# Kernel tuning notes

Hardware: AMD Instinct MI355X
Metric: run time of the kernel (lower is better)

The kernel has to match this reference:

```python
import jax, jax.numpy as jnp
import numpy as np

ND, NT, B = 16384, 16384, 4096
FD, FT, C = 256, 256, 768


def _gat(x_src, x_dst, ei, Ws, Wd, a_s, a_d, b, num_dst, self_loops):
    """PyG GATConv, heads=1: per-edge attention softmax over incoming edges."""
    if self_loops:
        loops = jnp.arange(num_dst, dtype=ei.dtype)
        ei = jnp.concatenate([ei, jnp.stack([loops, loops])], axis=1)
    src, dst = ei[0], ei[1]
    hs = x_src @ Ws                                   # [Ns, C]
    hd = x_dst @ Wd                                   # [Ndst, C]
    e = jax.nn.leaky_relu((hs @ a_s)[src] + (hd @ a_d)[dst], 0.2)   # [E]
    m = jax.ops.segment_max(e, dst, num_segments=num_dst)
    p = jnp.exp(e - m[dst])
    s = jax.ops.segment_sum(p, dst, num_segments=num_dst)
    alpha = p / (s[dst] + 1e-16)
    out = jax.ops.segment_sum(hs[src] * alpha[:, None], dst, num_segments=num_dst)
    return out + b


def _l2norm(x):
    n = jnp.linalg.norm(x, axis=1, keepdims=True)
    return x / jnp.maximum(n, 1e-12)


def setup_inputs() -> dict:
    ks = iter(jax.random.split(jax.random.key(0), 64))
    def nrm(shape, fan_in=None):
        s = 1.0 if fan_in is None else (1.0 / fan_in) ** 0.5
        return jax.random.normal(next(ks), shape, jnp.float32) * s
    inp = {}
    inp["x_drug"] = nrm((ND, FD))
    inp["x_target"] = nrm((NT, FT))
    inp["cell_features"] = nrm((B, 890))
    for et, fs, fd in (("dd", FD, FD), ("dt", FD, FT), ("tt", FT, FT)):
        inp[f"W_src_{et}"] = nrm((fs, C), fs)
        inp[f"W_dst_{et}"] = nrm((fd, C), fd)
        inp[f"a_src_{et}"] = nrm((C,), C)
        inp[f"a_dst_{et}"] = nrm((C,), C)
        inp[f"b_{et}"] = jnp.zeros((C,), jnp.float32)
    for name, fi, fo in (("red1", 890, 2048), ("red2", 2048, 512), ("red3", 512, 2 * C),
                         ("r2a", 4 * C, 2048), ("r2b", 2048, 512), ("r2c", 512, C), ("cls", C, 2)):
        inp[f"{name}_w"] = nrm((fi, fo), fi)
        inp[f"{name}_b"] = jnp.zeros((fo,), jnp.float32)
    inp["drug1_id"] = jax.random.randint(next(ks), (B,), 0, ND)
    inp["drug2_id"] = jax.random.randint(next(ks), (B,), 0, ND)
    inp["ei_dd"] = jax.random.randint(next(ks), (2, 131072), 0, ND)
    inp["ei_dt"] = jnp.stack([jax.random.randint(next(ks), (262144,), 0, ND),
                              jax.random.randint(next(ks), (262144,), 0, NT)])
    inp["ei_tt"] = jax.random.randint(next(ks), (2, 262144), 0, NT)
    return inp


def reference(x_drug, x_target, cell_features,
              W_src_dd, W_dst_dd, a_src_dd, a_dst_dd, b_dd,
              W_src_dt, W_dst_dt, a_src_dt, a_dst_dt, b_dt,
              W_src_tt, W_dst_tt, a_src_tt, a_dst_tt, b_tt,
              red1_w, red1_b, red2_w, red2_b, red3_w, red3_b,
              r2a_w, r2a_b, r2b_w, r2b_b, r2c_w, r2c_b,
              cls_w, cls_b,
              drug1_id, drug2_id, ei_dd, ei_dt, ei_tt):
    # HeteroConv (aggr='sum') followed by per-type ReLU, num_layers=1
    drug = jax.nn.relu(_gat(x_drug, x_drug, ei_dd,
                            W_src_dd, W_dst_dd, a_src_dd, a_dst_dd, b_dd, ND, True))
    target = jax.nn.relu(
        _gat(x_drug, x_target, ei_dt, W_src_dt, W_dst_dt, a_src_dt, a_dst_dt, b_dt, NT, False)
        + _gat(x_target, x_target, ei_tt, W_src_tt, W_dst_tt, a_src_tt, a_dst_tt, b_tt, NT, True))
    del target  # with num_layers=1 the target embeddings never feed the output (faithful)
    d1 = drug[drug1_id]
    d2 = drug[drug2_id]
    cell = _l2norm(cell_features)
    cell = jax.nn.relu(cell @ red1_w + red1_b)
    cell = jax.nn.relu(cell @ red2_w + red2_b)
    cell = jax.nn.relu(cell @ red3_w + red3_b)          # [B, 2*C]
    hidden = _l2norm(jnp.concatenate([d1, d2, cell], axis=1))  # [B, 4*C]
    hidden = jax.nn.relu(hidden @ r2a_w + r2a_b)
    hidden = jax.nn.relu(hidden @ r2b_w + r2b_b)
    hidden = jax.nn.relu(hidden @ r2c_w + r2c_b)
    return hidden @ cls_w + cls_b                       # [B, 2]
```

## Files before the change

kernel.cpp:

```cpp
#include <hip/hip_runtime.h>
#include <cstdint>

#define ND 16384
#define BATCH 4096
#define CDIM 768
#define E_DD 131072
#define FD 256

typedef unsigned short u16;
typedef u16 u16x4 __attribute__((ext_vector_type(4)));
typedef u16 u16x8 __attribute__((ext_vector_type(8)));
typedef short s16x8 __attribute__((ext_vector_type(8)));
typedef float f32x4 __attribute__((ext_vector_type(4)));

__device__ __forceinline__ u16 f2bf(float x) {
  union { float f; uint32_t u; } v; v.f = x;
  uint32_t r = v.u + 0x7fffu + ((v.u >> 16) & 1u);
  return (u16)(r >> 16);
}
__device__ __forceinline__ float bf2f(u16 h) {
  union { float f; uint32_t u; } v; v.u = ((uint32_t)h) << 16;
  return v.f;
}
__device__ __forceinline__ uint32_t split2p(float x) {
  u16 h = f2bf(x);
  u16 l = f2bf(x - bf2f(h));
  return ((uint32_t)h << 16) | l;
}

#define GLOAD_LDS16(gp, lp)                                                   \
  __builtin_amdgcn_global_load_lds(                                           \
      (__attribute__((address_space(1))) void*)(gp),                          \
      (__attribute__((address_space(3))) void*)(lp), 16, 0, 0)

#define KP 40

template <int KS, int OUT_BF16, int RELU, int BIAS, int ASPLIT, int ALO, int BLO,
          int BKD>
__device__ __forceinline__ void gemm_core(
    int bx, int by, int bz,
    const float* __restrict__ Af,
    const u16* __restrict__ Ahi, const u16* __restrict__ Alo,
    const u16* __restrict__ Bhi, const u16* __restrict__ Blo,
    const float* __restrict__ bias,
    float* __restrict__ Cf, u16* __restrict__ Chi,
    int M, int N, int K, u16* AsB, u16* BsB) {
  constexpr int MT = 4, NT = 4;
  constexpr int BM = 128, BN = 128;
  constexpr int ASEG = BM / 64;
  constexpr int BSEG = BN / 64;
  constexpr bool DIRECT = (ASPLIT == 0 && ALO == 0 && BLO == 0);

  const int t = threadIdx.x;
  const int bm0 = bx * BM, bn0 = by * BN;
  const int wid = t >> 6, lane = t & 63;
  const int quad = lane >> 4, l16 = lane & 15;
  const int wm0 = (wid >> 1) * (MT * 16);
  const int wn0 = (wid & 1) * (NT * 16);

  const int chunk = K / KS;
  const int kbeg = (KS > 1) ? bz * chunk : 0;
  const int kend = kbeg + chunk;

  f32x4 acc[MT][NT];
#pragma unroll
  for (int i = 0; i < MT; ++i)
#pragma unroll
    for (int j = 0; j < NT; ++j) acc[i][j] = (f32x4){0.f, 0.f, 0.f, 0.f};

  if constexpr (DIRECT) {
    constexpr int SLOTS = BKD / 8;
    constexpr int SM = SLOTS - 1;
    constexpr int NLD = (BM * BKD) / (256 * 8);
    auto stageA = [&](int buf, int kk) {
#pragma unroll
      for (int c = 0; c < NLD; ++c) {
        int s = t + 256 * c;
        int r = s / SLOTS, j = s % SLOTS;
        int jj = j ^ (r & SM);
        size_t goff = (size_t)(bm0 + r) * K + kk + jj * 8;
        int lofs = __builtin_amdgcn_readfirstlane((wid * 64 + 256 * c) * 8);
        GLOAD_LDS16(Ahi + goff, AsB + buf * (BM * BKD) + lofs);
      }
    };
    auto stageB = [&](int buf, int kk) {
#pragma unroll
      for (int c = 0; c < NLD; ++c) {
        int s = t + 256 * c;
        int r = s / SLOTS, j = s % SLOTS;
        int jj = j ^ (r & SM);
        size_t goff = (size_t)(bn0 + r) * K + kk + jj * 8;
        int lofs = __builtin_amdgcn_readfirstlane((wid * 64 + 256 * c) * 8);
        GLOAD_LDS16(Bhi + goff, BsB + buf * (BN * BKD) + lofs);
      }
    };
    stageA(0, kbeg);
    stageB(0, kbeg);
    const int rsw = l16 & SM;
    int cur = 0;
    for (int k0 = kbeg;;) {
      __syncthreads();
      int kn = k0 + BKD;
      if (kn < kend) {
        stageA(cur ^ 1, kn);
        stageB(cur ^ 1, kn);
      }
      const u16* Ab = AsB + cur * (BM * BKD);
      const u16* Bb = BsB + cur * (BN * BKD);
#pragma unroll
      for (int h = 0; h < BKD / 32; ++h) {
        s16x8 ah[MT], bh[NT];
#pragma unroll
        for (int mi = 0; mi < MT; ++mi)
          ah[mi] = *(const s16x8*)(Ab + (wm0 + mi * 16 + l16) * BKD +
                                   (((h * 4 + quad) ^ rsw) * 8));
#pragma unroll
        for (int ni = 0; ni < NT; ++ni)
          bh[ni] = *(const s16x8*)(Bb + (wn0 + ni * 16 + l16) * BKD +
                                   (((h * 4 + quad) ^ rsw) * 8));
#pragma unroll
        for (int mi = 0; mi < MT; ++mi)
#pragma unroll
          for (int ni = 0; ni < NT; ++ni)
            acc[mi][ni] = __builtin_amdgcn_mfma_f32_16x16x32_bf16(
                ah[mi], bh[ni], acc[mi][ni], 0, 0, 0);
      }
      k0 = kn;
      cur ^= 1;
      if (k0 >= kend) break;
    }
  } else {
    auto As = [&](int a, int r, int k) -> u16& { return AsB[(a * BM + r) * KP + k]; };
    auto Bs = [&](int a, int r, int k) -> u16& { return BsB[(a * BN + r) * KP + k]; };

    u16x8 pAh[ASEG], pAl[ASEG], pBh[BSEG], pBl[BSEG];

    auto loadA = [&](int c, int kk) {
      int s = t + 256 * c, row = s >> 2, kq = (s & 3) * 8;
      size_t off = (size_t)(bm0 + row) * K + kk + kq;
      if (ASPLIT) {
        f32x4 v0 = *(const f32x4*)(Af + off);
        f32x4 v1 = *(const f32x4*)(Af + off + 4);
        u16x8 h, l;
#pragma unroll
        for (int e = 0; e < 4; ++e) {
          uint32_t p = split2p(v0[e]);
          h[e] = (u16)(p >> 16); l[e] = (u16)(p & 0xffffu);
          uint32_t q = split2p(v1[e]);
          h[e + 4] = (u16)(q >> 16); l[e + 4] = (u16)(q & 0xffffu);
        }
        pAh[c] = h; pAl[c] = l;
      } else {
        pAh[c] = *(const u16x8*)(Ahi + off);
        if (ALO) pAl[c] = *(const u16x8*)(Alo + off);
      }
    };
    auto loadB = [&](int c, int kk) {
      int s = t + 256 * c, row = s >> 2, kq = (s & 3) * 8;
      size_t off = (size_t)(bn0 + row) * K + kk + kq;
      pBh[c] = *(const u16x8*)(Bhi + off);
      if (BLO) pBl[c] = *(const u16x8*)(Blo + off);
    };

#pragma unroll
    for (int c = 0; c < ASEG; ++c) loadA(c, kbeg);
#pragma unroll
    for (int c = 0; c < BSEG; ++c) loadB(c, kbeg);

    for (int k0 = kbeg;;) {
      __syncthreads();
#pragma unroll
      for (int c = 0; c < ASEG; ++c) {
        int s = t + 256 * c, row = s >> 2, kq = (s & 3) * 8;
        *(u16x8*)&As(0, row, kq) = pAh[c];
        if (ALO) *(u16x8*)&As(1, row, kq) = pAl[c];
      }
#pragma unroll
      for (int c = 0; c < BSEG; ++c) {
        int s = t + 256 * c, row = s >> 2, kq = (s & 3) * 8;
        *(u16x8*)&Bs(0, row, kq) = pBh[c];
        if (BLO) *(u16x8*)&Bs(1, row, kq) = pBl[c];
      }
      __syncthreads();

      int kn = k0 + 32;
      if (kn < kend) {
#pragma unroll
        for (int c = 0; c < ASEG; ++c) loadA(c, kn);
#pragma unroll
        for (int c = 0; c < BSEG; ++c) loadB(c, kn);
      }

      s16x8 ah[MT], al[MT], bh[NT], bl[NT];
#pragma unroll
      for (int mi = 0; mi < MT; ++mi) {
        ah[mi] = *(const s16x8*)&As(0, wm0 + mi * 16 + l16, quad * 8);
        if (ALO) al[mi] = *(const s16x8*)&As(1, wm0 + mi * 16 + l16, quad * 8);
      }
#pragma unroll
      for (int ni = 0; ni < NT; ++ni) {
        bh[ni] = *(const s16x8*)&Bs(0, wn0 + ni * 16 + l16, quad * 8);
        if (BLO) bl[ni] = *(const s16x8*)&Bs(1, wn0 + ni * 16 + l16, quad * 8);
      }
#pragma unroll
      for (int mi = 0; mi < MT; ++mi)
#pragma unroll
        for (int ni = 0; ni < NT; ++ni) {
          acc[mi][ni] = __builtin_amdgcn_mfma_f32_16x16x32_bf16(
              ah[mi], bh[ni], acc[mi][ni], 0, 0, 0);
          if (BLO)
            acc[mi][ni] = __builtin_amdgcn_mfma_f32_16x16x32_bf16(
                ah[mi], bl[ni], acc[mi][ni], 0, 0, 0);
          if (ALO)
            acc[mi][ni] = __builtin_amdgcn_mfma_f32_16x16x32_bf16(
                al[mi], bh[ni], acc[mi][ni], 0, 0, 0);
        }
      k0 = kn;
      if (k0 >= kend) break;
    }
  }

  float* Cp = (KS > 1) ? Cf + (size_t)bz * M * N : Cf;
#pragma unroll
  for (int mi = 0; mi < MT; ++mi) {
#pragma unroll
    for (int ni = 0; ni < NT; ++ni) {
      int row = bm0 + wm0 + mi * 16 + quad * 4;
      int col = bn0 + wn0 + ni * 16 + l16;
      float bv = BIAS ? bias[col] : 0.f;
#pragma unroll
      for (int r = 0; r < 4; ++r) {
        float v = acc[mi][ni][r] + bv;
        if (RELU) v = fmaxf(v, 0.f);
        size_t o = (size_t)(row + r) * N + col;
        if (OUT_BF16) Chi[o] = f2bf(v);
        else Cp[o] = v;
      }
    }
  }
}

template <int KS, int OUT_BF16, int RELU, int BIAS, int ASPLIT, int ALO, int BLO,
          int BKD>
__global__ __launch_bounds__(256) void mfma_gemm(
    const float* __restrict__ Af,
    const u16* __restrict__ Ahi, const u16* __restrict__ Alo,
    const u16* __restrict__ Bhi, const u16* __restrict__ Blo,
    const float* __restrict__ bias,
    float* __restrict__ Cf, u16* __restrict__ Chi,
    int M, int N, int K) {
  constexpr bool DIRECT = (ASPLIT == 0 && ALO == 0 && BLO == 0);
  __shared__ __align__(16) u16 AsB[DIRECT ? 2 * 128 * BKD : (ALO ? 2 : 1) * 128 * KP];
  __shared__ __align__(16) u16 BsB[DIRECT ? 2 * 128 * BKD : (BLO ? 2 : 1) * 128 * KP];
  gemm_core<KS, OUT_BF16, RELU, BIAS, ASPLIT, ALO, BLO, BKD>(
      blockIdx.x, blockIdx.y, (KS > 1) ? (int)blockIdx.z : 0,
      Af, Ahi, Alo, Bhi, Blo, bias, Cf, Chi, M, N, K, AsB, BsB);
}

__global__ __launch_bounds__(256) void dual_gemm_red1_hs(
    const u16* __restrict__ cn, const u16* __restrict__ r1T,
    const float* __restrict__ red1_b, u16* __restrict__ c1,
    const float* __restrict__ xd, const u16* __restrict__ wsrcT,
    u16* __restrict__ hs) {
  __shared__ __align__(16) u16 SMEM[16384];
  int b = blockIdx.x;
  if (b < 512) {
    gemm_core<1, 1, 1, 1, 0, 0, 0, 32>(b & 31, b >> 5, 0, nullptr, cn, nullptr,
                                       r1T, nullptr, red1_b, nullptr, c1,
                                       BATCH, 2048, 896, SMEM, SMEM + 2 * 128 * 32);
  } else {
    int b2 = b - 512;
    gemm_core<1, 1, 0, 0, 1, 1, 0, 32>(b2 & 127, b2 >> 7, 0, xd, nullptr, nullptr,
                                       wsrcT, nullptr, nullptr, nullptr, hs,
                                       ND, CDIM, FD, SMEM, SMEM + 2 * 128 * KP);
  }
}

template <int KS>
__global__ void reduce_split_ks(const float* __restrict__ P,
                                const float* __restrict__ bias,
                                u16* __restrict__ Chi, int M, int N) {
  int i = blockIdx.x * 256 + threadIdx.x;
  int total = (M * N) >> 2;
  if (i >= total) return;
  f32x4 s = ((const f32x4*)P)[i];
#pragma unroll
  for (int z = 1; z < KS; ++z) s += ((const f32x4*)P)[(size_t)z * total + i];
  int col = (i * 4) % N;
  f32x4 bv = *(const f32x4*)(bias + col);
  u16x4 h;
#pragma unroll
  for (int e = 0; e < 4; ++e) h[e] = f2bf(fmaxf(s[e] + bv[e], 0.f));
  *(u16x4*)&Chi[i * 4] = h;
}

__global__ void reduce_cls(const float* __restrict__ P,
                           const float* __restrict__ bias,
                           const float* __restrict__ clsw,
                           const float* __restrict__ clsb,
                           float* __restrict__ out) {
  int row = blockIdx.x * 4 + (threadIdx.x >> 6);
  int lane = threadIdx.x & 63;
  const f32x4* p0 = (const f32x4*)(P + (size_t)row * CDIM);
  const f32x4* p1 = (const f32x4*)(P + (size_t)BATCH * CDIM + (size_t)row * CDIM);
  float s0 = 0.f, s1 = 0.f;
#pragma unroll
  for (int i = 0; i < 3; ++i) {
    int c4 = lane + 64 * i;
    f32x4 a = p0[c4] + p1[c4];
    f32x4 bv = *(const f32x4*)(bias + c4 * 4);
#pragma unroll
    for (int e = 0; e < 4; ++e) {
      float h = fmaxf(a[e] + bv[e], 0.f);
      int c = c4 * 4 + e;
      s0 = fmaf(h, clsw[c * 2 + 0], s0);
      s1 = fmaf(h, clsw[c * 2 + 1], s1);
    }
  }
#pragma unroll
  for (int m = 32; m; m >>= 1) {
    s0 += __shfl_xor(s0, m);
    s1 += __shfl_xor(s1, m);
  }
  if (lane == 0) {
    out[row * 2 + 0] = s0 + clsb[0];
    out[row * 2 + 1] = s1 + clsb[1];
  }
}

struct TDesc {
  const float* W;
  u16* Th;
  int K, N, Kpad, start;
};
struct TPack { TDesc d[7]; };

__global__ void multi_transpose(TPack p) {
  __shared__ float tile[32][33];
  int b = blockIdx.x;
  int mi = 0;
#pragma unroll
  for (int i = 1; i < 7; ++i)
    if (b >= p.d[i].start) mi = i;
  TDesc dd = p.d[mi];
  int rel = b - dd.start;
  int tilesX = dd.Kpad / 32;
  int k0 = (rel % tilesX) * 32, n0 = (rel / tilesX) * 32;
  int tx = threadIdx.x, ty = threadIdx.y;
#pragma unroll
  for (int i = 0; i < 4; ++i) {
    int k = k0 + ty + 8 * i, n = n0 + tx;
    tile[ty + 8 * i][tx] = (k < dd.K && n < dd.N) ? dd.W[(size_t)k * dd.N + n] : 0.f;
  }
  __syncthreads();
#pragma unroll
  for (int i = 0; i < 4; ++i) {
    int n = n0 + ty + 8 * i, k = k0 + tx;
    if (n < dd.N) dd.Th[(size_t)n * dd.Kpad + k] = f2bf(tile[tx][ty + 8 * i]);
  }
}

__global__ void wvec_kernel(const float* __restrict__ Wsrc,
                            const float* __restrict__ Wdst,
                            const float* __restrict__ a_s,
                            const float* __restrict__ a_d,
                            float* __restrict__ wsv, float* __restrict__ wdv) {
  int k = blockIdx.x;
  int t = threadIdx.x;
  __shared__ float rs[256], rd[256];
  float s = 0.f, d = 0.f;
  for (int c = t; c < CDIM; c += 256) {
    s += Wsrc[(size_t)k * CDIM + c] * a_s[c];
    d += Wdst[(size_t)k * CDIM + c] * a_d[c];
  }
  rs[t] = s; rd[t] = d;
  __syncthreads();
  for (int st = 128; st; st >>= 1) {
    if (t < st) { rs[t] += rs[t + st]; rd[t] += rd[t + st]; }
    __syncthreads();
  }
  if (t == 0) { wsv[k] = rs[0]; wdv[k] = rd[0]; }
}

__global__ void esed_kernel(const float* __restrict__ x,
                            const float* __restrict__ wsv,
                            const float* __restrict__ wdv,
                            float* __restrict__ es, float* __restrict__ ed) {
  int i = blockIdx.x * 256 + threadIdx.x;
  int lane = threadIdx.x & 63;
  int row = i >> 6;
  int c4 = lane * 4;
  f32x4 v = ((const f32x4*)x)[i];
  f32x4 ws = *(const f32x4*)(wsv + c4);
  f32x4 wd = *(const f32x4*)(wdv + c4);
  float a = v[0] * ws[0] + v[1] * ws[1] + v[2] * ws[2] + v[3] * ws[3];
  float b = v[0] * wd[0] + v[1] * wd[1] + v[2] * wd[2] + v[3] * wd[3];
#pragma unroll
  for (int m = 32; m; m >>= 1) {
    a += __shfl_xor(a, m);
    b += __shfl_xor(b, m);
  }
  if (lane == 0) { es[row] = a; ed[row] = b; }
}

__global__ void init_csr(int* counts, int* mask, int* cnt) {
  int i = blockIdx.x * 256 + threadIdx.x;
  if (i < ND) { counts[i] = 1; mask[i] = 0; }
  if (i == 0) *cnt = 0;
}
__global__ void mark_kernel(const int* __restrict__ d1, const int* __restrict__ d2,
                            int* mask) {
  int i = blockIdx.x * 256 + threadIdx.x;
  if (i < BATCH) {
    mask[d1[i]] = 1;
    mask[d2[i]] = 1;
  }
}
__global__ void compact_kernel(const int* __restrict__ mask, int* cnt, int* list) {
  int i = blockIdx.x * 256 + threadIdx.x;
  if (i < ND && mask[i]) {
    int pos = atomicAdd(cnt, 1);
    list[pos] = i;
  }
}

__global__ void count_edges(const int* __restrict__ dst, int* counts) {
  int e = blockIdx.x * 256 + threadIdx.x;
  if (e < E_DD) atomicAdd(&counts[dst[e]], 1);
}
__global__ void scan_kernel(const int* __restrict__ counts, int* __restrict__ offsets,
                            int* __restrict__ cursor, int* __restrict__ slots) {
  __shared__ int part[512];
  int t = threadIdx.x;
  int base = t * 32;
  int s = 0;
  for (int i = 0; i < 32; ++i) s += counts[base + i];
  part[t] = s;
  __syncthreads();
  if (t == 0) {
    int run = 0;
    for (int i = 0; i < 512; ++i) { int tmp = part[i]; part[i] = run; run += tmp; }
    offsets[ND] = run;
  }
  __syncthreads();
  int run = part[t];
  for (int i = 0; i < 32; ++i) {
    int d = base + i;
    offsets[d] = run;
    slots[run] = d;
    cursor[d] = run + 1;
    run += counts[d];
  }
}
__global__ void scatter_edges(const int* __restrict__ src, const int* __restrict__ dst,
                              int* cursor, int* slots) {
  int e = blockIdx.x * 256 + threadIdx.x;
  if (e < E_DD) {
    int pos = atomicAdd(&cursor[dst[e]], 1);
    slots[pos] = src[e];
  }
}

__global__ __launch_bounds__(256) void gat_aggregate(
    const u16* __restrict__ hs, const float* __restrict__ es,
    const float* __restrict__ ed, const int* __restrict__ offsets,
    const int* __restrict__ slots, const float* __restrict__ bias,
    const int* __restrict__ list, const int* __restrict__ cnt,
    u16* __restrict__ out) {
  int idx = blockIdx.x * 4 + (threadIdx.x >> 6);
  if (idx >= *cnt) return;
  int d = list[idx];
  int lane = threadIdx.x & 63;
  int beg = offsets[d], end = offsets[d + 1];
  float edv = ed[d];
  float mx = -1e30f;
  for (int j = beg + lane; j < end; j += 64) {
    float e = es[slots[j]] + edv;
    e = e >= 0.f ? e : 0.2f * e;
    mx = fmaxf(mx, e);
  }
#pragma unroll
  for (int m = 32; m; m >>= 1) mx = fmaxf(mx, __shfl_xor(mx, m));
  float sm = 0.f;
  for (int j = beg + lane; j < end; j += 64) {
    float e = es[slots[j]] + edv;
    e = e >= 0.f ? e : 0.2f * e;
    sm += expf(e - mx);
  }
#pragma unroll
  for (int m = 32; m; m >>= 1) sm += __shfl_xor(sm, m);
  float inv = 1.f / (sm + 1e-16f);
  int c8 = lane * 8;
  int c4 = 512 + lane * 4;
  float a8[8] = {};
  float a4[4] = {};
  for (int j = beg; j < end; ++j) {
    int srcn = slots[j];
    float e = es[srcn] + edv;
    e = e >= 0.f ? e : 0.2f * e;
    float alpha = expf(e - mx) * inv;
    const u16* hrow = hs + (size_t)srcn * CDIM;
    u16x8 r8 = *(const u16x8*)(hrow + c8);
    u16x4 r4 = *(const u16x4*)(hrow + c4);
#pragma unroll
    for (int e2 = 0; e2 < 8; ++e2) a8[e2] = fmaf(alpha, bf2f(r8[e2]), a8[e2]);
#pragma unroll
    for (int e2 = 0; e2 < 4; ++e2) a4[e2] = fmaf(alpha, bf2f(r4[e2]), a4[e2]);
  }
  u16* orow = out + (size_t)d * CDIM;
  u16x8 o8;
  u16x4 o4;
#pragma unroll
  for (int e2 = 0; e2 < 8; ++e2) o8[e2] = f2bf(fmaxf(a8[e2] + bias[c8 + e2], 0.f));
#pragma unroll
  for (int e2 = 0; e2 < 4; ++e2) o4[e2] = f2bf(fmaxf(a4[e2] + bias[c4 + e2], 0.f));
  *(u16x8*)(orow + c8) = o8;
  *(u16x4*)(orow + c4) = o4;
}

__global__ void l2norm_bf16(const float* __restrict__ in, u16* __restrict__ hi,
                            int L, int Lp) {
  int row = blockIdx.x;
  int t = threadIdx.x;
  __shared__ float red[256];
  const float* irow = in + (size_t)row * L;
  float s = 0.f;
  for (int c = t; c < L; c += 256) { float v = irow[c]; s += v * v; }
  red[t] = s;
  __syncthreads();
  for (int st = 128; st; st >>= 1) {
    if (t < st) red[t] += red[t + st];
    __syncthreads();
  }
  float inv = 1.f / fmaxf(sqrtf(red[0]), 1e-12f);
  for (int c = t; c < Lp; c += 256) {
    float v = (c < L) ? irow[c] * inv : 0.f;
    hi[(size_t)row * Lp + c] = f2bf(v);
  }
}

__global__ __launch_bounds__(256) void hidden_build_bf16(
    const u16* __restrict__ drug, const u16* __restrict__ c3,
    const int* __restrict__ d1, const int* __restrict__ d2,
    u16* __restrict__ hhi) {
  int row = blockIdx.x;
  int t = threadIdx.x;
  const u16* s1 = drug + (size_t)d1[row] * CDIM;
  const u16* s2 = drug + (size_t)d2[row] * CDIM;
  const u16* s3 = c3 + (size_t)row * (2 * CDIM);
  float vals[12];
  float ss = 0.f;
#pragma unroll
  for (int i = 0; i < 12; ++i) {
    int c = t + 256 * i;
    float v;
    if (i < 3)      v = bf2f(s1[c]);
    else if (i < 6) v = bf2f(s2[c - CDIM]);
    else            v = bf2f(s3[c - 2 * CDIM]);
    vals[i] = v;
    ss += v * v;
  }
  __shared__ float red[256];
  red[t] = ss;
  __syncthreads();
  for (int st = 128; st; st >>= 1) {
    if (t < st) red[t] += red[t + st];
    __syncthreads();
  }
  float inv = 1.f / fmaxf(sqrtf(red[0]), 1e-12f);
  u16* hrow_h = hhi + (size_t)row * (4 * CDIM);
#pragma unroll
  for (int i = 0; i < 12; ++i) hrow_h[t + 256 * i] = f2bf(vals[i] * inv);
}

extern "C" void kernel_launch(void* const* d_in, const int* in_sizes, int n_in,
                              void* d_out, int out_size, void* d_ws, size_t ws_size,
                              hipStream_t stream) {
  const float* x_drug   = (const float*)d_in[0];
  const float* cellf    = (const float*)d_in[2];
  const float* W_src_dd = (const float*)d_in[3];
  const float* W_dst_dd = (const float*)d_in[4];
  const float* a_src_dd = (const float*)d_in[5];
  const float* a_dst_dd = (const float*)d_in[6];
  const float* b_dd     = (const float*)d_in[7];
  const float* red1_w = (const float*)d_in[18];
  const float* red1_b = (const float*)d_in[19];
  const float* red2_w = (const float*)d_in[20];
  const float* red2_b = (const float*)d_in[21];
  const float* red3_w = (const float*)d_in[22];
  const float* red3_b = (const float*)d_in[23];
  const float* r2a_w  = (const float*)d_in[24];
  const float* r2a_b  = (const float*)d_in[25];
  const float* r2b_w  = (const float*)d_in[26];
  const float* r2b_b  = (const float*)d_in[27];
  const float* r2c_w  = (const float*)d_in[28];
  const float* r2c_b  = (const float*)d_in[29];
  const float* cls_w  = (const float*)d_in[30];
  const float* cls_b  = (const float*)d_in[31];
  const int* drug1_id = (const int*)d_in[32];
  const int* drug2_id = (const int*)d_in[33];
  const int* ei_dd    = (const int*)d_in[34];
  float* out = (float*)d_out;

  const int* dd_src = ei_dd;
  const int* dd_dst = ei_dd + E_DD;

  char* w = (char*)d_ws;
  size_t off = 0;
  auto alloc = [&](size_t bytes) -> char* {
    char* p = w + off;
    off = (off + bytes + 255) & ~(size_t)255;
    return p;
  };
  u16* hs   = (u16*)alloc((size_t)ND * CDIM * 2);
  u16* drug = (u16*)alloc((size_t)ND * CDIM * 2);
  u16* c3   = (u16*)alloc((size_t)BATCH * 2 * CDIM * 2);
  float* P  = (float*)alloc((size_t)4 * BATCH * 512 * 4);
  u16* hid_hi = hs;
  u16* cn_hi = (u16*)alloc((size_t)BATCH * 896 * 2);
  u16* c1_hi = (u16*)alloc((size_t)BATCH * 2048 * 2);
  u16* c2_hi = (u16*)alloc((size_t)BATCH * 512 * 2);
  u16* wsrcT_hi = (u16*)alloc((size_t)CDIM * FD * 2);
  u16* r1T_hi = (u16*)alloc((size_t)2048 * 896 * 2);
  u16* r2T_hi = (u16*)alloc((size_t)512 * 2048 * 2);
  u16* r3T_hi = (u16*)alloc((size_t)1536 * 512 * 2);
  u16* raT_hi = (u16*)alloc((size_t)2048 * 3072 * 2);
  u16* rbT_hi = (u16*)alloc((size_t)512 * 2048 * 2);
  u16* rcT_hi = (u16*)alloc((size_t)768 * 512 * 2);
  float* es  = (float*)alloc((size_t)ND * 4);
  float* ed  = (float*)alloc((size_t)ND * 4);
  float* wsv = (float*)alloc(FD * 4);
  float* wdv = (float*)alloc(FD * 4);
  int* counts  = (int*)alloc((size_t)ND * 4);
  int* offsets = (int*)alloc((size_t)(ND + 1) * 4);
  int* cursor  = (int*)alloc((size_t)ND * 4);
  int* slots   = (int*)alloc((size_t)(E_DD + ND) * 4);
  int* mask    = (int*)alloc((size_t)ND * 4);
  int* list    = (int*)alloc((size_t)ND * 4);
  int* cnt     = (int*)alloc(256);
  (void)ws_size; (void)n_in; (void)in_sizes; (void)out_size;

  TPack tp;
  tp.d[0] = {W_src_dd, wsrcT_hi, 256, 768, 256, 0};
  tp.d[1] = {red1_w, r1T_hi, 890, 2048, 896, 192};
  tp.d[2] = {red2_w, r2T_hi, 2048, 512, 2048, 1984};
  tp.d[3] = {red3_w, r3T_hi, 512, 1536, 512, 3008};
  tp.d[4] = {r2a_w, raT_hi, 3072, 2048, 3072, 3776};
  tp.d[5] = {r2b_w, rbT_hi, 2048, 512, 2048, 9920};
  tp.d[6] = {r2c_w, rcT_hi, 512, 768, 512, 10944};
  multi_transpose<<<11328, dim3(32, 8), 0, stream>>>(tp);

  wvec_kernel<<<FD, 256, 0, stream>>>(W_src_dd, W_dst_dd, a_src_dd, a_dst_dd, wsv, wdv);
  esed_kernel<<<ND * FD / 1024, 256, 0, stream>>>(x_drug, wsv, wdv, es, ed);
  init_csr<<<ND / 256, 256, 0, stream>>>(counts, mask, cnt);
  mark_kernel<<<BATCH / 256, 256, 0, stream>>>(drug1_id, drug2_id, mask);
  compact_kernel<<<ND / 256, 256, 0, stream>>>(mask, cnt, list);
  l2norm_bf16<<<BATCH, 256, 0, stream>>>(cellf, cn_hi, 890, 896);

  dual_gemm_red1_hs<<<1280, 256, 0, stream>>>(cn_hi, r1T_hi, red1_b, c1_hi,
                                              x_drug, wsrcT_hi, hs);

  mfma_gemm<4, 0, 0, 0, 0, 0, 0, 64><<<dim3(BATCH / 128, 512 / 128, 4), 256, 0, stream>>>(
      nullptr, c1_hi, nullptr, r2T_hi, nullptr, nullptr, P, nullptr, BATCH, 512, 2048);
  reduce_split_ks<4><<<BATCH * 512 / 1024, 256, 0, stream>>>(P, red2_b, c2_hi, BATCH, 512);
  mfma_gemm<1, 1, 1, 1, 0, 0, 0, 64><<<dim3(BATCH / 128, 1536 / 128), 256, 0, stream>>>(
      nullptr, c2_hi, nullptr, r3T_hi, nullptr, red3_b, nullptr, c3, BATCH, 1536, 512);

  count_edges<<<E_DD / 256, 256, 0, stream>>>(dd_dst, counts);
  scan_kernel<<<1, 512, 0, stream>>>(counts, offsets, cursor, slots);
  scatter_edges<<<E_DD / 256, 256, 0, stream>>>(dd_src, dd_dst, cursor, slots);
  gat_aggregate<<<ND / 4, 256, 0, stream>>>(hs, es, ed, offsets, slots, b_dd, list, cnt, drug);

  hidden_build_bf16<<<BATCH, 256, 0, stream>>>(drug, c3, drug1_id, drug2_id, hid_hi);

  mfma_gemm<1, 1, 1, 1, 0, 0, 0, 64><<<dim3(BATCH / 128, 2048 / 128), 256, 0, stream>>>(
      nullptr, hid_hi, nullptr, raT_hi, nullptr, r2a_b, nullptr, c1_hi, BATCH, 2048, 3072);
  mfma_gemm<4, 0, 0, 0, 0, 0, 0, 64><<<dim3(BATCH / 128, 512 / 128, 4), 256, 0, stream>>>(
      nullptr, c1_hi, nullptr, rbT_hi, nullptr, nullptr, P, nullptr, BATCH, 512, 2048);
  reduce_split_ks<4><<<BATCH * 512 / 1024, 256, 0, stream>>>(P, r2b_b, c2_hi, BATCH, 512);
  mfma_gemm<2, 0, 0, 0, 0, 0, 0, 64><<<dim3(BATCH / 128, CDIM / 128, 2), 256, 0, stream>>>(
      nullptr, c2_hi, nullptr, rcT_hi, nullptr, nullptr, P, nullptr, BATCH, CDIM, 512);
  reduce_cls<<<BATCH / 4, 256, 0, stream>>>(P, r2c_b, cls_w, cls_b, out);
}
```

Before: 461.3 us.

## Add 4-stage counted-vmcnt LDS pipeline for direct bf16 GEMMs

Adds a 4-buffer, BK=32 pipeline path to the direct-load MFMA GEMM. It issues three stages ahead and waits with explicit s_waitcnt vmcnt counts instead of a full __syncthreads drain, so global-to-LDS loads overlap compute more deeply. All standalone dense GEMM launches switch from 2x64 to 4x32 buffering, keeping LDS size the same. Bias loads are also hoisted before the main loop. The hand-counted vmcnt depends on the exact number of loads each stage issues, which makes it fragile, and the smaller K step means more barriers per tile.

```diff
diff --git a/kernel.cpp b/kernel.cpp
--- a/kernel.cpp
+++ b/kernel.cpp
@@ -36,7 +36,7 @@
 #define KP 40
 
 template <int KS, int OUT_BF16, int RELU, int BIAS, int ASPLIT, int ALO, int BLO,
-          int BKD>
+          int BKD, int NBUF>
 __device__ __forceinline__ void gemm_core(
     int bx, int by, int bz,
     const float* __restrict__ Af,
@@ -62,6 +62,11 @@
   const int kbeg = (KS > 1) ? bz * chunk : 0;
   const int kend = kbeg + chunk;
 
+  float bvv[NT];
+#pragma unroll
+  for (int ni = 0; ni < NT; ++ni)
+    bvv[ni] = BIAS ? bias[bn0 + wn0 + ni * 16 + l16] : 0.f;
+
   f32x4 acc[MT][NT];
 #pragma unroll
   for (int i = 0; i < MT; ++i)
@@ -94,30 +99,71 @@
         GLOAD_LDS16(Bhi + goff, BsB + buf * (BN * BKD) + lofs);
       }
     };
-    stageA(0, kbeg);
-    stageB(0, kbeg);
     const int rsw = l16 & SM;
-    int cur = 0;
-    for (int k0 = kbeg;;) {
-      __syncthreads();
-      int kn = k0 + BKD;
-      if (kn < kend) {
-        stageA(cur ^ 1, kn);
-        stageB(cur ^ 1, kn);
-      }
-      const u16* Ab = AsB + cur * (BM * BKD);
-      const u16* Bb = BsB + cur * (BN * BKD);
-#pragma unroll
-      for (int h = 0; h < BKD / 32; ++h) {
+
+    if constexpr (NBUF == 2) {
+      stageA(0, kbeg);
+      stageB(0, kbeg);
+      int cur = 0;
+      for (int k0 = kbeg;;) {
+        __syncthreads();
+        int kn = k0 + BKD;
+        if (kn < kend) {
+          stageA(cur ^ 1, kn);
+          stageB(cur ^ 1, kn);
+        }
+        const u16* Ab = AsB + cur * (BM * BKD);
+        const u16* Bb = BsB + cur * (BN * BKD);
+#pragma unroll
+        for (int h = 0; h < BKD / 32; ++h) {
+          s16x8 ah[MT], bh[NT];
+#pragma unroll
+          for (int mi = 0; mi < MT; ++mi)
+            ah[mi] = *(const s16x8*)(Ab + (wm0 + mi * 16 + l16) * BKD +
+                                     (((h * 4 + quad) ^ rsw) * 8));
+#pragma unroll
+          for (int ni = 0; ni < NT; ++ni)
+            bh[ni] = *(const s16x8*)(Bb + (wn0 + ni * 16 + l16) * BKD +
+                                     (((h * 4 + quad) ^ rsw) * 8));
+#pragma unroll
+          for (int mi = 0; mi < MT; ++mi)
+#pragma unroll
+            for (int ni = 0; ni < NT; ++ni)
+              acc[mi][ni] = __builtin_amdgcn_mfma_f32_16x16x32_bf16(
+                  ah[mi], bh[ni], acc[mi][ni], 0, 0, 0);
+        }
+        k0 = kn;
+        cur ^= 1;
+        if (k0 >= kend) break;
+      }
+    } else {
+      static_assert(NBUF == 4 && BKD == 32, "counted path assumes 4x32");
+      const int nt = (kend - kbeg) / BKD;
+      stageA(0, kbeg);            stageB(0, kbeg);
+      stageA(1, kbeg + BKD);      stageB(1, kbeg + BKD);
+      stageA(2, kbeg + 2 * BKD);  stageB(2, kbeg + 2 * BKD);
+      for (int i = 0; i < nt; ++i) {
+        if (i <= nt - 3)      asm volatile("s_waitcnt vmcnt(8)" ::: "memory");
+        else if (i == nt - 2) asm volatile("s_waitcnt vmcnt(4)" ::: "memory");
+        else                  asm volatile("s_waitcnt vmcnt(0)" ::: "memory");
+        __builtin_amdgcn_s_barrier();
+        __builtin_amdgcn_sched_barrier(0);
+        if (i + 3 < nt) {
+          int b = (i + 3) & 3, kk = kbeg + (i + 3) * BKD;
+          stageA(b, kk);
+          stageB(b, kk);
+        }
+        const u16* Ab = AsB + (i & 3) * (BM * BKD);
+        const u16* Bb = BsB + (i & 3) * (BM * BKD);
         s16x8 ah[MT], bh[NT];
 #pragma unroll
         for (int mi = 0; mi < MT; ++mi)
           ah[mi] = *(const s16x8*)(Ab + (wm0 + mi * 16 + l16) * BKD +
-                                   (((h * 4 + quad) ^ rsw) * 8));
+                                   ((quad ^ rsw) * 8));
 #pragma unroll
         for (int ni = 0; ni < NT; ++ni)
           bh[ni] = *(const s16x8*)(Bb + (wn0 + ni * 16 + l16) * BKD +
-                                   (((h * 4 + quad) ^ rsw) * 8));
+                                   ((quad ^ rsw) * 8));
 #pragma unroll
         for (int mi = 0; mi < MT; ++mi)
 #pragma unroll
@@ -125,9 +171,6 @@
             acc[mi][ni] = __builtin_amdgcn_mfma_f32_16x16x32_bf16(
                 ah[mi], bh[ni], acc[mi][ni], 0, 0, 0);
       }
-      k0 = kn;
-      cur ^= 1;
-      if (k0 >= kend) break;
     }
   } else {
     auto As = [&](int a, int r, int k) -> u16& { return AsB[(a * BM + r) * KP + k]; };
@@ -227,10 +270,9 @@
     for (int ni = 0; ni < NT; ++ni) {
       int row = bm0 + wm0 + mi * 16 + quad * 4;
       int col = bn0 + wn0 + ni * 16 + l16;
-      float bv = BIAS ? bias[col] : 0.f;
 #pragma unroll
       for (int r = 0; r < 4; ++r) {
-        float v = acc[mi][ni][r] + bv;
+        float v = acc[mi][ni][r] + bvv[ni];
         if (RELU) v = fmaxf(v, 0.f);
         size_t o = (size_t)(row + r) * N + col;
         if (OUT_BF16) Chi[o] = f2bf(v);
@@ -241,7 +283,7 @@
 }
 
 template <int KS, int OUT_BF16, int RELU, int BIAS, int ASPLIT, int ALO, int BLO,
-          int BKD>
+          int BKD, int NBUF>
 __global__ __launch_bounds__(256) void mfma_gemm(
     const float* __restrict__ Af,
     const u16* __restrict__ Ahi, const u16* __restrict__ Alo,
@@ -250,9 +292,9 @@
     float* __restrict__ Cf, u16* __restrict__ Chi,
     int M, int N, int K) {
   constexpr bool DIRECT = (ASPLIT == 0 && ALO == 0 && BLO == 0);
-  __shared__ __align__(16) u16 AsB[DIRECT ? 2 * 128 * BKD : (ALO ? 2 : 1) * 128 * KP];
-  __shared__ __align__(16) u16 BsB[DIRECT ? 2 * 128 * BKD : (BLO ? 2 : 1) * 128 * KP];
-  gemm_core<KS, OUT_BF16, RELU, BIAS, ASPLIT, ALO, BLO, BKD>(
+  __shared__ __align__(16) u16 AsB[DIRECT ? NBUF * 128 * BKD : (ALO ? 2 : 1) * 128 * KP];
+  __shared__ __align__(16) u16 BsB[DIRECT ? NBUF * 128 * BKD : (BLO ? 2 : 1) * 128 * KP];
+  gemm_core<KS, OUT_BF16, RELU, BIAS, ASPLIT, ALO, BLO, BKD, NBUF>(
       blockIdx.x, blockIdx.y, (KS > 1) ? (int)blockIdx.z : 0,
       Af, Ahi, Alo, Bhi, Blo, bias, Cf, Chi, M, N, K, AsB, BsB);
 }
@@ -265,14 +307,14 @@
   __shared__ __align__(16) u16 SMEM[16384];
   int b = blockIdx.x;
   if (b < 512) {
-    gemm_core<1, 1, 1, 1, 0, 0, 0, 32>(b & 31, b >> 5, 0, nullptr, cn, nullptr,
-                                       r1T, nullptr, red1_b, nullptr, c1,
-                                       BATCH, 2048, 896, SMEM, SMEM + 2 * 128 * 32);
+    gemm_core<1, 1, 1, 1, 0, 0, 0, 32, 2>(b & 31, b >> 5, 0, nullptr, cn, nullptr,
+                                          r1T, nullptr, red1_b, nullptr, c1,
+                                          BATCH, 2048, 896, SMEM, SMEM + 2 * 128 * 32);
   } else {
     int b2 = b - 512;
-    gemm_core<1, 1, 0, 0, 1, 1, 0, 32>(b2 & 127, b2 >> 7, 0, xd, nullptr, nullptr,
-                                       wsrcT, nullptr, nullptr, nullptr, hs,
-                                       ND, CDIM, FD, SMEM, SMEM + 2 * 128 * KP);
+    gemm_core<1, 1, 0, 0, 1, 1, 0, 32, 2>(b2 & 127, b2 >> 7, 0, xd, nullptr, nullptr,
+                                          wsrcT, nullptr, nullptr, nullptr, hs,
+                                          ND, CDIM, FD, SMEM, SMEM + 2 * 128 * KP);
   }
 }
 
@@ -660,10 +702,10 @@
   dual_gemm_red1_hs<<<1280, 256, 0, stream>>>(cn_hi, r1T_hi, red1_b, c1_hi,
                                               x_drug, wsrcT_hi, hs);
 
-  mfma_gemm<4, 0, 0, 0, 0, 0, 0, 64><<<dim3(BATCH / 128, 512 / 128, 4), 256, 0, stream>>>(
+  mfma_gemm<4, 0, 0, 0, 0, 0, 0, 32, 4><<<dim3(BATCH / 128, 512 / 128, 4), 256, 0, stream>>>(
       nullptr, c1_hi, nullptr, r2T_hi, nullptr, nullptr, P, nullptr, BATCH, 512, 2048);
   reduce_split_ks<4><<<BATCH * 512 / 1024, 256, 0, stream>>>(P, red2_b, c2_hi, BATCH, 512);
-  mfma_gemm<1, 1, 1, 1, 0, 0, 0, 64><<<dim3(BATCH / 128, 1536 / 128), 256, 0, stream>>>(
+  mfma_gemm<1, 1, 1, 1, 0, 0, 0, 32, 4><<<dim3(BATCH / 128, 1536 / 128), 256, 0, stream>>>(
       nullptr, c2_hi, nullptr, r3T_hi, nullptr, red3_b, nullptr, c3, BATCH, 1536, 512);
 
   count_edges<<<E_DD / 256, 256, 0, stream>>>(dd_dst, counts);
@@ -673,12 +715,12 @@
 
   hidden_build_bf16<<<BATCH, 256, 0, stream>>>(drug, c3, drug1_id, drug2_id, hid_hi);
 
-  mfma_gemm<1, 1, 1, 1, 0, 0, 0, 64><<<dim3(BATCH / 128, 2048 / 128), 256, 0, stream>>>(
+  mfma_gemm<1, 1, 1, 1, 0, 0, 0, 32, 4><<<dim3(BATCH / 128, 2048 / 128), 256, 0, stream>>>(
       nullptr, hid_hi, nullptr, raT_hi, nullptr, r2a_b, nullptr, c1_hi, BATCH, 2048, 3072);
-  mfma_gemm<4, 0, 0, 0, 0, 0, 0, 64><<<dim3(BATCH / 128, 512 / 128, 4), 256, 0, stream>>>(
+  mfma_gemm<4, 0, 0, 0, 0, 0, 0, 32, 4><<<dim3(BATCH / 128, 512 / 128, 4), 256, 0, stream>>>(
       nullptr, c1_hi, nullptr, rbT_hi, nullptr, nullptr, P, nullptr, BATCH, 512, 2048);
   reduce_split_ks<4><<<BATCH * 512 / 1024, 256, 0, stream>>>(P, r2b_b, c2_hi, BATCH, 512);
-  mfma_gemm<2, 0, 0, 0, 0, 0, 0, 64><<<dim3(BATCH / 128, CDIM / 128, 2), 256, 0, stream>>>(
+  mfma_gemm<2, 0, 0, 0, 0, 0, 0, 32, 4><<<dim3(BATCH / 128, CDIM / 128, 2), 256, 0, stream>>>(
       nullptr, c2_hi, nullptr, rcT_hi, nullptr, nullptr, P, nullptr, BATCH, CDIM, 512);
   reduce_cls<<<BATCH / 4, 256, 0, stream>>>(P, r2c_b, cls_w, cls_b, out);
 }
```

Measured after the change: 487.2 us. +5.6%, slower.

## Merge small preprocessing kernels into three block-dispatched prep launches

Applied to the files above, without the earlier changes.

Folds the weight transpose, weight-vector reduction, CSR initialisation, and cell L2-norm into one kernel that picks its role by block index. Edge-score computation, the drug mask marking and edge counting go into a second kernel, and compaction plus the prefix scan into a third. The CSR build is moved ahead of the GEMMs. This cuts about ten launches down to four, removing launch gaps and tail bubbles. The GEMM epilogue bias load is also hoisted before the main loop. Dependencies are kept by ordering the launches, though role-dispatched blocks may unbalance occupancy.

```diff
diff --git a/kernel.cpp b/kernel.cpp
--- a/kernel.cpp
+++ b/kernel.cpp
@@ -62,6 +62,11 @@
   const int kbeg = (KS > 1) ? bz * chunk : 0;
   const int kend = kbeg + chunk;
 
+  float bvv[NT];
+#pragma unroll
+  for (int ni = 0; ni < NT; ++ni)
+    bvv[ni] = BIAS ? bias[bn0 + wn0 + ni * 16 + l16] : 0.f;
+
   f32x4 acc[MT][NT];
 #pragma unroll
   for (int i = 0; i < MT; ++i)
@@ -94,9 +99,9 @@
         GLOAD_LDS16(Bhi + goff, BsB + buf * (BN * BKD) + lofs);
       }
     };
+    const int rsw = l16 & SM;
     stageA(0, kbeg);
     stageB(0, kbeg);
-    const int rsw = l16 & SM;
     int cur = 0;
     for (int k0 = kbeg;;) {
       __syncthreads();
@@ -227,10 +232,9 @@
     for (int ni = 0; ni < NT; ++ni) {
       int row = bm0 + wm0 + mi * 16 + quad * 4;
       int col = bn0 + wn0 + ni * 16 + l16;
-      float bv = BIAS ? bias[col] : 0.f;
 #pragma unroll
       for (int r = 0; r < 4; ++r) {
-        float v = acc[mi][ni][r] + bv;
+        float v = acc[mi][ni][r] + bvv[ni];
         if (RELU) v = fmaxf(v, 0.f);
         size_t o = (size_t)(row + r) * N + col;
         if (OUT_BF16) Chi[o] = f2bf(v);
@@ -335,123 +339,150 @@
 };
 struct TPack { TDesc d[7]; };
 
-__global__ void multi_transpose(TPack p) {
-  __shared__ float tile[32][33];
+#define P1_T 11328
+#define P1_W (P1_T + 256)
+#define P1_I (P1_W + 64)
+__global__ __launch_bounds__(256) void prep1(
+    TPack p,
+    const float* __restrict__ Wsrc, const float* __restrict__ Wdst,
+    const float* __restrict__ a_s, const float* __restrict__ a_d,
+    float* __restrict__ wsv, float* __restrict__ wdv,
+    int* __restrict__ counts, int* __restrict__ mask, int* __restrict__ cnt,
+    const float* __restrict__ cellf, u16* __restrict__ cn_hi) {
+  __shared__ __align__(16) float S[1088];
   int b = blockIdx.x;
-  int mi = 0;
-#pragma unroll
-  for (int i = 1; i < 7; ++i)
-    if (b >= p.d[i].start) mi = i;
-  TDesc dd = p.d[mi];
-  int rel = b - dd.start;
-  int tilesX = dd.Kpad / 32;
-  int k0 = (rel % tilesX) * 32, n0 = (rel / tilesX) * 32;
-  int tx = threadIdx.x, ty = threadIdx.y;
-#pragma unroll
-  for (int i = 0; i < 4; ++i) {
-    int k = k0 + ty + 8 * i, n = n0 + tx;
-    tile[ty + 8 * i][tx] = (k < dd.K && n < dd.N) ? dd.W[(size_t)k * dd.N + n] : 0.f;
-  }
-  __syncthreads();
-#pragma unroll
-  for (int i = 0; i < 4; ++i) {
-    int n = n0 + ty + 8 * i, k = k0 + tx;
-    if (n < dd.N) dd.Th[(size_t)n * dd.Kpad + k] = f2bf(tile[tx][ty + 8 * i]);
-  }
-}
-
-__global__ void wvec_kernel(const float* __restrict__ Wsrc,
-                            const float* __restrict__ Wdst,
-                            const float* __restrict__ a_s,
-                            const float* __restrict__ a_d,
-                            float* __restrict__ wsv, float* __restrict__ wdv) {
-  int k = blockIdx.x;
   int t = threadIdx.x;
-  __shared__ float rs[256], rd[256];
-  float s = 0.f, d = 0.f;
-  for (int c = t; c < CDIM; c += 256) {
-    s += Wsrc[(size_t)k * CDIM + c] * a_s[c];
-    d += Wdst[(size_t)k * CDIM + c] * a_d[c];
-  }
-  rs[t] = s; rd[t] = d;
-  __syncthreads();
-  for (int st = 128; st; st >>= 1) {
-    if (t < st) { rs[t] += rs[t + st]; rd[t] += rd[t + st]; }
+  if (b < P1_T) {
+    float (*tile)[33] = (float(*)[33])S;
+    int mi = 0;
+#pragma unroll
+    for (int i = 1; i < 7; ++i)
+      if (b >= p.d[i].start) mi = i;
+    TDesc dd = p.d[mi];
+    int rel = b - dd.start;
+    int tilesX = dd.Kpad / 32;
+    int k0 = (rel % tilesX) * 32, n0 = (rel / tilesX) * 32;
+    int tx = t & 31, ty = t >> 5;
+#pragma unroll
+    for (int i = 0; i < 4; ++i) {
+      int k = k0 + ty + 8 * i, n = n0 + tx;
+      tile[ty + 8 * i][tx] = (k < dd.K && n < dd.N) ? dd.W[(size_t)k * dd.N + n] : 0.f;
+    }
     __syncthreads();
-  }
-  if (t == 0) { wsv[k] = rs[0]; wdv[k] = rd[0]; }
-}
-
-__global__ void esed_kernel(const float* __restrict__ x,
-                            const float* __restrict__ wsv,
-                            const float* __restrict__ wdv,
-                            float* __restrict__ es, float* __restrict__ ed) {
-  int i = blockIdx.x * 256 + threadIdx.x;
-  int lane = threadIdx.x & 63;
-  int row = i >> 6;
-  int c4 = lane * 4;
-  f32x4 v = ((const f32x4*)x)[i];
-  f32x4 ws = *(const f32x4*)(wsv + c4);
-  f32x4 wd = *(const f32x4*)(wdv + c4);
-  float a = v[0] * ws[0] + v[1] * ws[1] + v[2] * ws[2] + v[3] * ws[3];
-  float b = v[0] * wd[0] + v[1] * wd[1] + v[2] * wd[2] + v[3] * wd[3];
-#pragma unroll
-  for (int m = 32; m; m >>= 1) {
-    a += __shfl_xor(a, m);
-    b += __shfl_xor(b, m);
-  }
-  if (lane == 0) { es[row] = a; ed[row] = b; }
-}
-
-__global__ void init_csr(int* counts, int* mask, int* cnt) {
-  int i = blockIdx.x * 256 + threadIdx.x;
-  if (i < ND) { counts[i] = 1; mask[i] = 0; }
-  if (i == 0) *cnt = 0;
-}
-__global__ void mark_kernel(const int* __restrict__ d1, const int* __restrict__ d2,
-                            int* mask) {
-  int i = blockIdx.x * 256 + threadIdx.x;
-  if (i < BATCH) {
+#pragma unroll
+    for (int i = 0; i < 4; ++i) {
+      int n = n0 + ty + 8 * i, k = k0 + tx;
+      if (n < dd.N) dd.Th[(size_t)n * dd.Kpad + k] = f2bf(tile[tx][ty + 8 * i]);
+    }
+  } else if (b < P1_W) {
+    int k = b - P1_T;
+    float* rs = S;
+    float* rd = S + 256;
+    float s = 0.f, d = 0.f;
+    for (int c = t; c < CDIM; c += 256) {
+      s += Wsrc[(size_t)k * CDIM + c] * a_s[c];
+      d += Wdst[(size_t)k * CDIM + c] * a_d[c];
+    }
+    rs[t] = s; rd[t] = d;
+    __syncthreads();
+    for (int st = 128; st; st >>= 1) {
+      if (t < st) { rs[t] += rs[t + st]; rd[t] += rd[t + st]; }
+      __syncthreads();
+    }
+    if (t == 0) { wsv[k] = rs[0]; wdv[k] = rd[0]; }
+  } else if (b < P1_I) {
+    int i = (b - P1_W) * 256 + t;
+    if (i < ND) { counts[i] = 1; mask[i] = 0; }
+    if (i == 0) *cnt = 0;
+  } else {
+    int row = b - P1_I;
+    float* red = S;
+    const float* irow = cellf + (size_t)row * 890;
+    float s = 0.f;
+    for (int c = t; c < 890; c += 256) { float v = irow[c]; s += v * v; }
+    red[t] = s;
+    __syncthreads();
+    for (int st = 128; st; st >>= 1) {
+      if (t < st) red[t] += red[t + st];
+      __syncthreads();
+    }
+    float inv = 1.f / fmaxf(sqrtf(red[0]), 1e-12f);
+    for (int c = t; c < 896; c += 256) {
+      float v = (c < 890) ? irow[c] * inv : 0.f;
+      cn_hi[(size_t)row * 896 + c] = f2bf(v);
+    }
+  }
+}
+
+#define P2_E (ND * FD / 1024)
+#define P2_M (P2_E + BATCH / 256)
+__global__ __launch_bounds__(256) void prep2(
+    const float* __restrict__ x, const float* __restrict__ wsv,
+    const float* __restrict__ wdv, float* __restrict__ es, float* __restrict__ ed,
+    const int* __restrict__ d1, const int* __restrict__ d2, int* __restrict__ mask,
+    const int* __restrict__ dst, int* __restrict__ counts) {
+  int b = blockIdx.x, t = threadIdx.x;
+  if (b < P2_E) {
+    int i = b * 256 + t;
+    int lane = t & 63;
+    int row = i >> 6;
+    int c4 = lane * 4;
+    f32x4 v = ((const f32x4*)x)[i];
+    f32x4 ws = *(const f32x4*)(wsv + c4);
+    f32x4 wd = *(const f32x4*)(wdv + c4);
+    float a = v[0] * ws[0] + v[1] * ws[1] + v[2] * ws[2] + v[3] * ws[3];
+    float bb = v[0] * wd[0] + v[1] * wd[1] + v[2] * wd[2] + v[3] * wd[3];
+#pragma unroll
+    for (int m = 32; m; m >>= 1) {
+      a += __shfl_xor(a, m);
+      bb += __shfl_xor(bb, m);
+    }
+    if (lane == 0) { es[row] = a; ed[row] = bb; }
+  } else if (b < P2_M) {
+    int i = (b - P2_E) * 256 + t;
     mask[d1[i]] = 1;
     mask[d2[i]] = 1;
-  }
-}
-__global__ void compact_kernel(const int* __restrict__ mask, int* cnt, int* list) {
-  int i = blockIdx.x * 256 + threadIdx.x;
-  if (i < ND && mask[i]) {
-    int pos = atomicAdd(cnt, 1);
-    list[pos] = i;
-  }
-}
-
-__global__ void count_edges(const int* __restrict__ dst, int* counts) {
-  int e = blockIdx.x * 256 + threadIdx.x;
-  if (e < E_DD) atomicAdd(&counts[dst[e]], 1);
-}
-__global__ void scan_kernel(const int* __restrict__ counts, int* __restrict__ offsets,
-                            int* __restrict__ cursor, int* __restrict__ slots) {
+  } else {
+    int e = (b - P2_M) * 256 + t;
+    atomicAdd(&counts[dst[e]], 1);
+  }
+}
+
+__global__ __launch_bounds__(512) void prep3(
+    const int* __restrict__ mask, int* __restrict__ cnt, int* __restrict__ list,
+    const int* __restrict__ counts, int* __restrict__ offsets,
+    int* __restrict__ cursor, int* __restrict__ slots) {
   __shared__ int part[512];
-  int t = threadIdx.x;
-  int base = t * 32;
-  int s = 0;
-  for (int i = 0; i < 32; ++i) s += counts[base + i];
-  part[t] = s;
-  __syncthreads();
-  if (t == 0) {
-    int run = 0;
-    for (int i = 0; i < 512; ++i) { int tmp = part[i]; part[i] = run; run += tmp; }
-    offsets[ND] = run;
-  }
-  __syncthreads();
-  int run = part[t];
-  for (int i = 0; i < 32; ++i) {
-    int d = base + i;
-    offsets[d] = run;
-    slots[run] = d;
-    cursor[d] = run + 1;
-    run += counts[d];
-  }
-}
+  int b = blockIdx.x, t = threadIdx.x;
+  if (b < 32) {
+    int i = b * 512 + t;
+    if (mask[i]) {
+      int pos = atomicAdd(cnt, 1);
+      list[pos] = i;
+    }
+  } else {
+    int base = t * 32;
+    int s = 0;
+    for (int i = 0; i < 32; ++i) s += counts[base + i];
+    part[t] = s;
+    __syncthreads();
+    if (t == 0) {
+      int run = 0;
+      for (int i = 0; i < 512; ++i) { int tmp = part[i]; part[i] = run; run += tmp; }
+      offsets[ND] = run;
+    }
+    __syncthreads();
+    int run = part[t];
+    for (int i = 0; i < 32; ++i) {
+      int d = base + i;
+      offsets[d] = run;
+      slots[run] = d;
+      cursor[d] = run + 1;
+      run += counts[d];
+    }
+  }
+}
+
 __global__ void scatter_edges(const int* __restrict__ src, const int* __restrict__ dst,
                               int* cursor, int* slots) {
   int e = blockIdx.x * 256 + threadIdx.x;
@@ -516,27 +547,6 @@
   for (int e2 = 0; e2 < 4; ++e2) o4[e2] = f2bf(fmaxf(a4[e2] + bias[c4 + e2], 0.f));
   *(u16x8*)(orow + c8) = o8;
   *(u16x4*)(orow + c4) = o4;
-}
-
-__global__ void l2norm_bf16(const float* __restrict__ in, u16* __restrict__ hi,
-                            int L, int Lp) {
-  int row = blockIdx.x;
-  int t = threadIdx.x;
-  __shared__ float red[256];
-  const float* irow = in + (size_t)row * L;
-  float s = 0.f;
-  for (int c = t; c < L; c += 256) { float v = irow[c]; s += v * v; }
-  red[t] = s;
-  __syncthreads();
-  for (int st = 128; st; st >>= 1) {
-    if (t < st) red[t] += red[t + st];
-    __syncthreads();
-  }
-  float inv = 1.f / fmaxf(sqrtf(red[0]), 1e-12f);
-  for (int c = t; c < Lp; c += 256) {
-    float v = (c < L) ? irow[c] * inv : 0.f;
-    hi[(size_t)row * Lp + c] = f2bf(v);
-  }
 }
 
 __global__ __launch_bounds__(256) void hidden_build_bf16(
@@ -648,14 +658,14 @@
   tp.d[4] = {r2a_w, raT_hi, 3072, 2048, 3072, 3776};
   tp.d[5] = {r2b_w, rbT_hi, 2048, 512, 2048, 9920};
   tp.d[6] = {r2c_w, rcT_hi, 512, 768, 512, 10944};
-  multi_transpose<<<11328, dim3(32, 8), 0, stream>>>(tp);
-
-  wvec_kernel<<<FD, 256, 0, stream>>>(W_src_dd, W_dst_dd, a_src_dd, a_dst_dd, wsv, wdv);
-  esed_kernel<<<ND * FD / 1024, 256, 0, stream>>>(x_drug, wsv, wdv, es, ed);
-  init_csr<<<ND / 256, 256, 0, stream>>>(counts, mask, cnt);
-  mark_kernel<<<BATCH / 256, 256, 0, stream>>>(drug1_id, drug2_id, mask);
-  compact_kernel<<<ND / 256, 256, 0, stream>>>(mask, cnt, list);
-  l2norm_bf16<<<BATCH, 256, 0, stream>>>(cellf, cn_hi, 890, 896);
+  prep1<<<15744, 256, 0, stream>>>(tp, W_src_dd, W_dst_dd, a_src_dd, a_dst_dd,
+                                   wsv, wdv, counts, mask, cnt, cellf, cn_hi);
+
+  prep2<<<4624, 256, 0, stream>>>(x_drug, wsv, wdv, es, ed, drug1_id, drug2_id,
+                                  mask, dd_dst, counts);
+
+  prep3<<<33, 512, 0, stream>>>(mask, cnt, list, counts, offsets, cursor, slots);
+  scatter_edges<<<E_DD / 256, 256, 0, stream>>>(dd_src, dd_dst, cursor, slots);
 
   dual_gemm_red1_hs<<<1280, 256, 0, stream>>>(cn_hi, r1T_hi, red1_b, c1_hi,
                                               x_drug, wsrcT_hi, hs);
@@ -666,9 +676,6 @@
   mfma_gemm<1, 1, 1, 1, 0, 0, 0, 64><<<dim3(BATCH / 128, 1536 / 128), 256, 0, stream>>>(
       nullptr, c2_hi, nullptr, r3T_hi, nullptr, red3_b, nullptr, c3, BATCH, 1536, 512);
 
-  count_edges<<<E_DD / 256, 256, 0, stream>>>(dd_dst, counts);
-  scan_kernel<<<1, 512, 0, stream>>>(counts, offsets, cursor, slots);
-  scatter_edges<<<E_DD / 256, 256, 0, stream>>>(dd_src, dd_dst, cursor, slots);
   gat_aggregate<<<ND / 4, 256, 0, stream>>>(hs, es, ed, offsets, slots, b_dd, list, cnt, drug);
 
   hidden_build_bf16<<<BATCH, 256, 0, stream>>>(drug, c3, drug1_id, drug2_id, hid_hi);
```

Result: faster. 442.9 us (-4.0%).
